# Kernel optimization log

Measured on AMD Instinct MI355X. Metric: run time of the kernel, lower is better.

The kernel has to match this reference:

```python
import jax, jax.numpy as jnp
import numpy as np

N_NODES = 50000
NEG_SLOPE = 0.2  # PyG GATConv default
EPS = 1e-16      # PyG softmax denominator epsilon


def gat_conv(x, W, att_src, att_dst, bias, src, dst, heads, out_ch):
    # x: [N, F_in]; W: [F_in, heads*out_ch]; att_*: [heads, out_ch]
    N = x.shape[0]
    h = (x @ W).reshape(N, heads, out_ch)              # [N,H,C]
    a_src = jnp.sum(h * att_src, axis=-1)              # [N,H]
    a_dst = jnp.sum(h * att_dst, axis=-1)              # [N,H]
    alpha = a_src[src] + a_dst[dst]                    # [E,H]
    alpha = jnp.where(alpha > 0, alpha, NEG_SLOPE * alpha)  # leaky_relu
    amax = jax.ops.segment_max(alpha, dst, num_segments=N)  # [N,H]
    amax = jnp.where(jnp.isfinite(amax), amax, 0.0)
    ex = jnp.exp(alpha - amax[dst])                    # [E,H]
    denom = jax.ops.segment_sum(ex, dst, num_segments=N)    # [N,H]
    coef = ex / (denom[dst] + EPS)                     # [E,H]
    msg = h[src] * coef[:, :, None]                    # [E,H,C]
    out = jax.ops.segment_sum(msg, dst, num_segments=N)     # [N,H,C]
    return out.reshape(N, heads * out_ch) + bias


def setup_inputs() -> dict:
    key = jax.random.key(0)
    ks = jax.random.split(key, 11)
    T, N, F = 8, N_NODES, 64
    E = 1_600_000
    x = jax.random.normal(ks[0], (T, N, F), dtype=jnp.float32)
    edge_index = jax.random.randint(ks[1], (2, E), 0, N, dtype=jnp.int64)
    s = 0.1
    return {
        "x": x,
        "edge_index": edge_index,
        "W1": jax.random.normal(ks[2], (F, 64), jnp.float32) * s,
        "att_src1": jax.random.normal(ks[3], (8, 8), jnp.float32) * s,
        "att_dst1": jax.random.normal(ks[4], (8, 8), jnp.float32) * s,
        "bias1": jax.random.normal(ks[5], (64,), jnp.float32) * s,
        "W2": jax.random.normal(ks[6], (64, F), jnp.float32) * s,
        "att_src2": jax.random.normal(ks[7], (1, F), jnp.float32) * s,
        "att_dst2": jax.random.normal(ks[8], (1, F), jnp.float32) * s,
        "bias2": jax.random.normal(ks[9], (F,), jnp.float32) * s,
    }


def reference(x, edge_index, W1, att_src1, att_dst1, bias1, W2, att_src2, att_dst2, bias2):
    N = x.shape[1]
    # PyG GATConv adds self-loops by default
    loops = jnp.arange(N, dtype=edge_index.dtype)
    src = jnp.concatenate([edge_index[0], loops])
    dst = jnp.concatenate([edge_index[1], loops])

    def step(xt):  # xt: [N, F] ; dropout is identity in eval mode
        y = jax.nn.elu(gat_conv(xt, W1, att_src1, att_dst1, bias1, src, dst, 8, 8))
        y = gat_conv(y, W2, att_src2, att_dst2, bias2, src, dst, 1, xt.shape[-1])
        return jax.nn.log_softmax(y, axis=-1)

    return jax.vmap(step)(x)  # [T, N, F]
```

## Files before the change

kernel.cpp:

```cpp
#include <hip/hip_runtime.h>
#include <hip/hip_bf16.h>
#include <math.h>


typedef __hip_bfloat16 bf16;

__device__ __forceinline__ float bf2f(unsigned short u) {
    return __uint_as_float(((unsigned int)u) << 16);
}


__global__ __launch_bounds__(256) void count_edges_kernel(const int* __restrict__ dsts,
                                                          int* cnt, int E) {
    int i = blockIdx.x * 256 + threadIdx.x;
    if (i < E) atomicAdd(&cnt[dsts[i]], 1);
}

__global__ __launch_bounds__(1024) void scan_kernel(const int* __restrict__ cnt,
                                                    int* row, int* cur, int N) {
    __shared__ int ls[1024];
    int t = threadIdx.x;
    int chunk = (N + 1023) / 1024;
    int b = t * chunk;
    int sum = 0;
    for (int i = 0; i < chunk; ++i) {
        int idx = b + i;
        if (idx < N) sum += cnt[idx] + 1;
    }
    ls[t] = sum;
    __syncthreads();
    for (int off = 1; off < 1024; off <<= 1) {
        int v = (t >= off) ? ls[t - off] : 0;
        __syncthreads();
        ls[t] += v;
        __syncthreads();
    }
    int run = (t == 0) ? 0 : ls[t - 1];
    for (int i = 0; i < chunk; ++i) {
        int idx = b + i;
        if (idx < N) {
            int c = cnt[idx] + 1;
            row[idx] = run;
            cur[idx] = run;
            run += c;
        }
    }
    if (t == 1023) row[N] = ls[1023];
}

__global__ __launch_bounds__(256) void fill_csr_kernel(const int* __restrict__ srcs,
                                                       const int* __restrict__ dsts,
                                                       int* cur, int* esrc, int E, int N) {
    int i = blockIdx.x * 256 + threadIdx.x;
    if (i >= E + N) return;
    int s, d;
    if (i < E) { s = srcs[i]; d = dsts[i]; }
    else       { s = i - E;   d = s; }
    int pos = atomicAdd(&cur[d], 1);
    esrc[pos] = s;
}


__device__ __forceinline__ float4 ld4(const float* p) { return *(const float4*)p; }
__device__ __forceinline__ float4 ld4(const bf16* p) {
    ushort4 u = *(const ushort4*)p;
    float4 r;
    r.x = bf2f(u.x); r.y = bf2f(u.y); r.z = bf2f(u.z); r.w = bf2f(u.w);
    return r;
}


template <typename TIN, int H, int C>
__global__ __launch_bounds__(256) void gemm_att_kernel(
    const TIN* __restrict__ xin,
    size_t node_stride, size_t t_stride,
    const float* __restrict__ Wm,
    const float* __restrict__ att_s,
    const float* __restrict__ att_d,
    bf16* __restrict__ hout,
    float* __restrict__ asrc,
    float* __restrict__ adst,
    int N) {
    __shared__ float Ws[64 * 64];
    int tid = threadIdx.x;
    {
        const float4* W4 = (const float4*)Wm;
        float4* Ws4 = (float4*)Ws;
#pragma unroll
        for (int i = 0; i < 4; ++i) Ws4[tid + 256 * i] = W4[tid + 256 * i];
    }
    __syncthreads();

    int c  = tid & 63;
    int wv = tid >> 6;
    int t0 = blockIdx.y * 4;
    int n  = blockIdx.x * 4 + wv;
    if (n >= N) return;

    const TIN* xb = xin + (size_t)n * node_stride + (size_t)t0 * t_stride;
    float acc[4] = {0.f, 0.f, 0.f, 0.f};

#pragma unroll 2
    for (int k4 = 0; k4 < 16; ++k4) {
        float4 xv[4];
#pragma unroll
        for (int r = 0; r < 4; ++r)
            xv[r] = ld4(xb + (size_t)r * t_stride + k4 * 4);
        float w0 = Ws[(4 * k4 + 0) * 64 + c];
        float w1 = Ws[(4 * k4 + 1) * 64 + c];
        float w2 = Ws[(4 * k4 + 2) * 64 + c];
        float w3 = Ws[(4 * k4 + 3) * 64 + c];
#pragma unroll
        for (int r = 0; r < 4; ++r) {
            acc[r] = fmaf(xv[r].x, w0, acc[r]);
            acc[r] = fmaf(xv[r].y, w1, acc[r]);
            acc[r] = fmaf(xv[r].z, w2, acc[r]);
            acc[r] = fmaf(xv[r].w, w3, acc[r]);
        }
    }

    float as_w = att_s[c];
    float ad_w = att_d[c];
    bf16*  hn  = hout + (size_t)n * 512;
    float* asn = asrc + (size_t)n * (8 * H);
    float* adn = adst + (size_t)n * (8 * H);
#pragma unroll
    for (int r = 0; r < 4; ++r) {
        int tt = t0 + r;
        float a = acc[r];
        hn[tt * 64 + c] = __float2bfloat16(a);
        float vs = a * as_w;
        float vd = a * ad_w;
#pragma unroll
        for (int off = 1; off < C; off <<= 1) {
            vs += __shfl_xor(vs, off, 64);
            vd += __shfl_xor(vd, off, 64);
        }
        if ((c % C) == 0) {
            int hd = c / C;
            asn[tt * H + hd] = vs;
            adn[tt * H + hd] = vd;
        }
    }
}


#define SWZ(PU, Q) __uint_as_float(__builtin_amdgcn_ds_swizzle((PU), ((Q) << 5) | 0x18))

template <int H, bool FINAL>
__global__ __launch_bounds__(256) void gat_edge_kernel(
    const bf16* __restrict__ h_all,
    const float* __restrict__ asrc_all,
    const float* __restrict__ adst_all,
    const int* __restrict__ row,
    const int* __restrict__ esrc,
    const float* __restrict__ bias,
    bf16* __restrict__ outb,
    float* __restrict__ outf,
    int N) {
    int tid  = threadIdx.x;
    int lane = tid & 63;
    int t0   = blockIdx.y * 4;
    int n    = blockIdx.x * 4 + (tid >> 6);
    if (n >= N) return;

    const char* asrcb = (const char*)asrc_all;
    const unsigned short* hb = (const unsigned short*)h_all;

    const int head = (H == 8) ? (lane >> 3) : 0;
    float adn[4];
#pragma unroll
    for (int i = 0; i < 4; ++i)
        adn[i] = adst_all[(size_t)n * (8 * H) + (t0 + i) * H + head];

    int e0  = row[n];
    int deg = row[n + 1] - e0;
    int toff = t0 * 64 + lane;

    float lsum[4] = {0.f, 0.f, 0.f, 0.f};
    float acc[4]  = {0.f, 0.f, 0.f, 0.f};

    for (int base = 0; base < deg; base += 64) {
        int cnt = deg - base; if (cnt > 64) cnt = 64;
        int sv = (lane < cnt) ? esrc[e0 + base + lane] : 0;

        if constexpr (H == 8) {
            unsigned head4 = (unsigned)(head << 2);
            unsigned l7_4  = (unsigned)((lane & 7) << 2);
#pragma unroll
            for (int sub = 0; sub < 8; ++sub) {
                if (sub * 8 >= cnt) break;
                int svj = __builtin_amdgcn_ds_bpermute(sub * 32 + l7_4, sv);
                unsigned abase = (((unsigned)svj) << 8) | head4;
                bool valid = (sub * 8 + (lane & 7) < cnt);
                float p[4];
#pragma unroll
                for (int i = 0; i < 4; ++i) {
                    float av = *(const float*)(asrcb + (abase | ((unsigned)(t0 + i) << 5)));
                    float tv = av + adn[i];
                    tv = tv > 0.f ? tv : 0.2f * tv;
                    tv = valid ? tv : -INFINITY;
                    p[i] = __expf(tv);
                    lsum[i] += p[i];
                }
                unsigned pu0 = __float_as_uint(p[0]);
                unsigned pu1 = __float_as_uint(p[1]);
                unsigned pu2 = __float_as_uint(p[2]);
                unsigned pu3 = __float_as_uint(p[3]);
#define ACC_EDGE(Q)                                                            \
    {                                                                          \
        unsigned sj = (unsigned)__builtin_amdgcn_readlane(sv, sub * 8 + (Q));  \
        const unsigned short* hrow = hb + ((size_t)sj << 9) + toff;            \
        acc[0] = fmaf(SWZ(pu0, Q), bf2f(hrow[0]),   acc[0]);                   \
        acc[1] = fmaf(SWZ(pu1, Q), bf2f(hrow[64]),  acc[1]);                   \
        acc[2] = fmaf(SWZ(pu2, Q), bf2f(hrow[128]), acc[2]);                   \
        acc[3] = fmaf(SWZ(pu3, Q), bf2f(hrow[192]), acc[3]);                   \
    }
                ACC_EDGE(0) ACC_EDGE(1) ACC_EDGE(2) ACC_EDGE(3)
                ACC_EDGE(4) ACC_EDGE(5) ACC_EDGE(6) ACC_EDGE(7)
#undef ACC_EDGE
            }
        } else {
            unsigned abase = ((unsigned)sv) << 5;
            float p[4];
#pragma unroll
            for (int i = 0; i < 4; ++i) {
                float av = *(const float*)(asrcb + (abase | ((unsigned)(t0 + i) << 2)));
                float tv = av + adn[i];
                tv = tv > 0.f ? tv : 0.2f * tv;
                tv = (lane < cnt) ? tv : -INFINITY;
                p[i] = __expf(tv);
                lsum[i] += p[i];
            }
            for (int j0 = 0; j0 < cnt; j0 += 8) {
#pragma unroll
                for (int q = 0; q < 8; ++q) {
                    int j = j0 + q;
                    unsigned sj = (unsigned)__builtin_amdgcn_readlane(sv, j);
                    const unsigned short* hrow = hb + ((size_t)sj << 9) + toff;
                    float pj0 = __uint_as_float(
                        __builtin_amdgcn_readlane(__float_as_uint(p[0]), j));
                    float pj1 = __uint_as_float(
                        __builtin_amdgcn_readlane(__float_as_uint(p[1]), j));
                    float pj2 = __uint_as_float(
                        __builtin_amdgcn_readlane(__float_as_uint(p[2]), j));
                    float pj3 = __uint_as_float(
                        __builtin_amdgcn_readlane(__float_as_uint(p[3]), j));
                    acc[0] = fmaf(pj0, bf2f(hrow[0]),   acc[0]);
                    acc[1] = fmaf(pj1, bf2f(hrow[64]),  acc[1]);
                    acc[2] = fmaf(pj2, bf2f(hrow[128]), acc[2]);
                    acc[3] = fmaf(pj3, bf2f(hrow[192]), acc[3]);
                }
            }
        }
    }

#pragma unroll
    for (int i = 0; i < 4; ++i) {
        float ls = lsum[i];
        if constexpr (H == 8) {
            ls += __shfl_xor(ls, 1, 64);
            ls += __shfl_xor(ls, 2, 64);
            ls += __shfl_xor(ls, 4, 64);
        } else {
#pragma unroll
            for (int o = 1; o < 64; o <<= 1) ls += __shfl_xor(ls, o, 64);
        }
        float v = acc[i] / (ls + 1e-16f) + bias[lane];
        if (!FINAL) {
            float y = v > 0.f ? v : expm1f(v);
            outb[(size_t)n * 512 + (t0 + i) * 64 + lane] = __float2bfloat16(y);
        } else {
            float mx = v;
#pragma unroll
            for (int off = 1; off < 64; off <<= 1) mx = fmaxf(mx, __shfl_xor(mx, off, 64));
            float ex = __expf(v - mx);
            float sm = ex;
#pragma unroll
            for (int off = 1; off < 64; off <<= 1) sm += __shfl_xor(sm, off, 64);
            outf[(size_t)(t0 + i) * N * 64 + (size_t)n * 64 + lane] =
                (v - mx) - __logf(sm);
        }
    }
}


extern "C" void kernel_launch(void* const* d_in, const int* in_sizes, int n_in,
                              void* d_out, int out_size, void* d_ws, size_t ws_size,
                              hipStream_t stream) {
    const float* x        = (const float*)d_in[0];
    const int*   eidx     = (const int*)d_in[1];
    const float* W1       = (const float*)d_in[2];
    const float* att_src1 = (const float*)d_in[3];
    const float* att_dst1 = (const float*)d_in[4];
    const float* bias1    = (const float*)d_in[5];
    const float* W2       = (const float*)d_in[6];
    const float* att_src2 = (const float*)d_in[7];
    const float* att_dst2 = (const float*)d_in[8];
    const float* bias2    = (const float*)d_in[9];
    float* dout = (float*)d_out;

    const int N = 50000;
    const int F = 64;
    const int E = in_sizes[1] / 2;
    const int T = in_sizes[0] / (N * F);
    const int NT = T * N;
    const int Etot = E + N;
    const int BPT = (N + 3) / 4;

    const int* srcs = eidx;
    const int* dsts = eidx + E;

    char* ws = (char*)d_ws;
    size_t off = 0;
    auto carve = [&](size_t bytes) -> void* {
        void* p = ws + off;
        off = (off + bytes + 255) & ~(size_t)255;
        return p;
    };
    bf16*  h_all  = (bf16*)carve((size_t)NT * 64 * sizeof(bf16));
    bf16*  y1_all = (bf16*)carve((size_t)NT * 64 * sizeof(bf16));
    float* asrc   = (float*)carve((size_t)NT * 8 * sizeof(float));
    float* adst   = (float*)carve((size_t)NT * 8 * sizeof(float));
    int*   rowp   = (int*)carve((size_t)(N + 1) * sizeof(int));
    int*   cnt    = (int*)carve((size_t)N * sizeof(int));
    int*   cur    = (int*)carve((size_t)N * sizeof(int));
    int*   esrc   = (int*)carve((size_t)Etot * sizeof(int));
    (void)ws_size;

    hipMemsetAsync(cnt, 0, (size_t)N * sizeof(int), stream);
    count_edges_kernel<<<(E + 255) / 256, 256, 0, stream>>>(dsts, cnt, E);
    scan_kernel<<<1, 1024, 0, stream>>>(cnt, rowp, cur, N);
    fill_csr_kernel<<<(E + N + 255) / 256, 256, 0, stream>>>(srcs, dsts, cur, esrc, E, N);

    dim3 ggrid((N + 3) / 4, 2);
    dim3 egrid(BPT, T / 4);
    gemm_att_kernel<float, 8, 8><<<ggrid, 256, 0, stream>>>(
        x, 64, (size_t)N * 64, W1, att_src1, att_dst1, h_all, asrc, adst, N);
    gat_edge_kernel<8, false><<<egrid, 256, 0, stream>>>(
        h_all, asrc, adst, rowp, esrc, bias1, y1_all, nullptr, N);
    gemm_att_kernel<bf16, 1, 64><<<ggrid, 256, 0, stream>>>(
        y1_all, 512, 64, W2, att_src2, att_dst2, h_all, asrc, adst, N);
    gat_edge_kernel<1, true><<<egrid, 256, 0, stream>>>(
        h_all, asrc, adst, rowp, esrc, bias2, nullptr, dout, N);
}
```

Measured before the change: 1.144 ms.

## Interleave timesteps in h layout and process all 8 timesteps per wave

The GEMM kernel now stores h as [node][channel][timestep] and attention scores as [node][head][timestep], so each lane loads one 16-byte vector per edge holding all 8 timesteps of its channel. The edge kernel drops the timestep grid dimension and handles all 8 timesteps in one wave. This halves the number of CSR traversals, esrc reads and readlanes per edge, and replaces scattered 2-byte gathers with 16-byte ones. The cost is doubled accumulator and probability register pressure, which may lower occupancy, and half as many blocks in flight.

```diff
diff --git a/kernel.cpp b/kernel.cpp
--- a/kernel.cpp
+++ b/kernel.cpp
@@ -7,6 +7,16 @@
 
 __device__ __forceinline__ float bf2f(unsigned short u) {
     return __uint_as_float(((unsigned int)u) << 16);
+}
+__device__ __forceinline__ float lo16(int u) {
+    return __uint_as_float(((unsigned)u) << 16);
+}
+__device__ __forceinline__ float hi16(int u) {
+    return __uint_as_float(((unsigned)u) & 0xFFFF0000u);
+}
+__device__ __forceinline__ unsigned short f2bfu(float f) {
+    bf16 b = __float2bfloat16(f);
+    return *reinterpret_cast<unsigned short*>(&b);
 }
 
 
@@ -119,16 +129,22 @@
         }
     }
 
+    {
+        unsigned short* hn = (unsigned short*)hout + (size_t)n * 512;
+        ushort4 hv;
+        hv.x = f2bfu(acc[0]); hv.y = f2bfu(acc[1]);
+        hv.z = f2bfu(acc[2]); hv.w = f2bfu(acc[3]);
+        *(ushort4*)(hn + c * 8 + t0) = hv;
+    }
+
     float as_w = att_s[c];
     float ad_w = att_d[c];
-    bf16*  hn  = hout + (size_t)n * 512;
-    float* asn = asrc + (size_t)n * (8 * H);
-    float* adn = adst + (size_t)n * (8 * H);
+    float* asn = asrc + (size_t)n * (H * 8);
+    float* adn = adst + (size_t)n * (H * 8);
 #pragma unroll
     for (int r = 0; r < 4; ++r) {
         int tt = t0 + r;
         float a = acc[r];
-        hn[tt * 64 + c] = __float2bfloat16(a);
         float vs = a * as_w;
         float vd = a * ad_w;
 #pragma unroll
@@ -138,8 +154,8 @@
         }
         if ((c % C) == 0) {
             int hd = c / C;
-            asn[tt * H + hd] = vs;
-            adn[tt * H + hd] = vd;
+            asn[hd * 8 + tt] = vs;
+            adn[hd * 8 + tt] = vd;
         }
     }
 }
@@ -160,104 +176,114 @@
     int N) {
     int tid  = threadIdx.x;
     int lane = tid & 63;
-    int t0   = blockIdx.y * 4;
     int n    = blockIdx.x * 4 + (tid >> 6);
     if (n >= N) return;
 
-    const char* asrcb = (const char*)asrc_all;
     const unsigned short* hb = (const unsigned short*)h_all;
-
     const int head = (H == 8) ? (lane >> 3) : 0;
-    float adn[4];
-#pragma unroll
-    for (int i = 0; i < 4; ++i)
-        adn[i] = adst_all[(size_t)n * (8 * H) + (t0 + i) * H + head];
+
+    float adn[8];
+    {
+        const float* adp = adst_all + (size_t)n * (H * 8) + (head << 3);
+        float4 d0 = ld4(adp), d1 = ld4(adp + 4);
+        adn[0] = d0.x; adn[1] = d0.y; adn[2] = d0.z; adn[3] = d0.w;
+        adn[4] = d1.x; adn[5] = d1.y; adn[6] = d1.z; adn[7] = d1.w;
+    }
 
     int e0  = row[n];
     int deg = row[n + 1] - e0;
-    int toff = t0 * 64 + lane;
-
-    float lsum[4] = {0.f, 0.f, 0.f, 0.f};
-    float acc[4]  = {0.f, 0.f, 0.f, 0.f};
+
+    float lsum[8] = {0.f, 0.f, 0.f, 0.f, 0.f, 0.f, 0.f, 0.f};
+    float acc[8]  = {0.f, 0.f, 0.f, 0.f, 0.f, 0.f, 0.f, 0.f};
 
     for (int base = 0; base < deg; base += 64) {
         int cnt = deg - base; if (cnt > 64) cnt = 64;
         int sv = (lane < cnt) ? esrc[e0 + base + lane] : 0;
 
         if constexpr (H == 8) {
-            unsigned head4 = (unsigned)(head << 2);
-            unsigned l7_4  = (unsigned)((lane & 7) << 2);
+            unsigned l7_4 = (unsigned)((lane & 7) << 2);
 #pragma unroll
             for (int sub = 0; sub < 8; ++sub) {
                 if (sub * 8 >= cnt) break;
                 int svj = __builtin_amdgcn_ds_bpermute(sub * 32 + l7_4, sv);
-                unsigned abase = (((unsigned)svj) << 8) | head4;
+                const float* ap = asrc_all + ((size_t)(unsigned)svj << 6) + (head << 3);
+                float4 a0 = ld4(ap), a1 = ld4(ap + 4);
                 bool valid = (sub * 8 + (lane & 7) < cnt);
-                float p[4];
-#pragma unroll
-                for (int i = 0; i < 4; ++i) {
-                    float av = *(const float*)(asrcb + (abase | ((unsigned)(t0 + i) << 5)));
-                    float tv = av + adn[i];
+                float at[8] = {a0.x, a0.y, a0.z, a0.w, a1.x, a1.y, a1.z, a1.w};
+                float p[8];
+#pragma unroll
+                for (int t = 0; t < 8; ++t) {
+                    float tv = at[t] + adn[t];
                     tv = tv > 0.f ? tv : 0.2f * tv;
                     tv = valid ? tv : -INFINITY;
-                    p[i] = __expf(tv);
-                    lsum[i] += p[i];
+                    p[t] = __expf(tv);
+                    lsum[t] += p[t];
                 }
-                unsigned pu0 = __float_as_uint(p[0]);
-                unsigned pu1 = __float_as_uint(p[1]);
-                unsigned pu2 = __float_as_uint(p[2]);
-                unsigned pu3 = __float_as_uint(p[3]);
+                unsigned pu0 = __float_as_uint(p[0]), pu1 = __float_as_uint(p[1]);
+                unsigned pu2 = __float_as_uint(p[2]), pu3 = __float_as_uint(p[3]);
+                unsigned pu4 = __float_as_uint(p[4]), pu5 = __float_as_uint(p[5]);
+                unsigned pu6 = __float_as_uint(p[6]), pu7 = __float_as_uint(p[7]);
 #define ACC_EDGE(Q)                                                            \
     {                                                                          \
         unsigned sj = (unsigned)__builtin_amdgcn_readlane(sv, sub * 8 + (Q));  \
-        const unsigned short* hrow = hb + ((size_t)sj << 9) + toff;            \
-        acc[0] = fmaf(SWZ(pu0, Q), bf2f(hrow[0]),   acc[0]);                   \
-        acc[1] = fmaf(SWZ(pu1, Q), bf2f(hrow[64]),  acc[1]);                   \
-        acc[2] = fmaf(SWZ(pu2, Q), bf2f(hrow[128]), acc[2]);                   \
-        acc[3] = fmaf(SWZ(pu3, Q), bf2f(hrow[192]), acc[3]);                   \
+        int4 hv = ((const int4*)(hb + ((size_t)sj << 9)))[lane];               \
+        acc[0] = fmaf(SWZ(pu0, Q), lo16(hv.x), acc[0]);                        \
+        acc[1] = fmaf(SWZ(pu1, Q), hi16(hv.x), acc[1]);                        \
+        acc[2] = fmaf(SWZ(pu2, Q), lo16(hv.y), acc[2]);                        \
+        acc[3] = fmaf(SWZ(pu3, Q), hi16(hv.y), acc[3]);                        \
+        acc[4] = fmaf(SWZ(pu4, Q), lo16(hv.z), acc[4]);                        \
+        acc[5] = fmaf(SWZ(pu5, Q), hi16(hv.z), acc[5]);                        \
+        acc[6] = fmaf(SWZ(pu6, Q), lo16(hv.w), acc[6]);                        \
+        acc[7] = fmaf(SWZ(pu7, Q), hi16(hv.w), acc[7]);                        \
     }
                 ACC_EDGE(0) ACC_EDGE(1) ACC_EDGE(2) ACC_EDGE(3)
                 ACC_EDGE(4) ACC_EDGE(5) ACC_EDGE(6) ACC_EDGE(7)
 #undef ACC_EDGE
             }
         } else {
-            unsigned abase = ((unsigned)sv) << 5;
-            float p[4];
-#pragma unroll
-            for (int i = 0; i < 4; ++i) {
-                float av = *(const float*)(asrcb + (abase | ((unsigned)(t0 + i) << 2)));
-                float tv = av + adn[i];
+            const float* ap = asrc_all + ((size_t)(unsigned)sv << 3);
+            float4 a0 = ld4(ap), a1 = ld4(ap + 4);
+            float at[8] = {a0.x, a0.y, a0.z, a0.w, a1.x, a1.y, a1.z, a1.w};
+            float p[8];
+#pragma unroll
+            for (int t = 0; t < 8; ++t) {
+                float tv = at[t] + adn[t];
                 tv = tv > 0.f ? tv : 0.2f * tv;
                 tv = (lane < cnt) ? tv : -INFINITY;
-                p[i] = __expf(tv);
-                lsum[i] += p[i];
+                p[t] = __expf(tv);
+                lsum[t] += p[t];
             }
             for (int j0 = 0; j0 < cnt; j0 += 8) {
 #pragma unroll
                 for (int q = 0; q < 8; ++q) {
                     int j = j0 + q;
                     unsigned sj = (unsigned)__builtin_amdgcn_readlane(sv, j);
-                    const unsigned short* hrow = hb + ((size_t)sj << 9) + toff;
-                    float pj0 = __uint_as_float(
-                        __builtin_amdgcn_readlane(__float_as_uint(p[0]), j));
-                    float pj1 = __uint_as_float(
-                        __builtin_amdgcn_readlane(__float_as_uint(p[1]), j));
-                    float pj2 = __uint_as_float(
-                        __builtin_amdgcn_readlane(__float_as_uint(p[2]), j));
-                    float pj3 = __uint_as_float(
-                        __builtin_amdgcn_readlane(__float_as_uint(p[3]), j));
-                    acc[0] = fmaf(pj0, bf2f(hrow[0]),   acc[0]);
-                    acc[1] = fmaf(pj1, bf2f(hrow[64]),  acc[1]);
-                    acc[2] = fmaf(pj2, bf2f(hrow[128]), acc[2]);
-                    acc[3] = fmaf(pj3, bf2f(hrow[192]), acc[3]);
+                    int4 hv = ((const int4*)(hb + ((size_t)sj << 9)))[lane];
+                    float pj0 = __uint_as_float(__builtin_amdgcn_readlane(__float_as_uint(p[0]), j));
+                    float pj1 = __uint_as_float(__builtin_amdgcn_readlane(__float_as_uint(p[1]), j));
+                    float pj2 = __uint_as_float(__builtin_amdgcn_readlane(__float_as_uint(p[2]), j));
+                    float pj3 = __uint_as_float(__builtin_amdgcn_readlane(__float_as_uint(p[3]), j));
+                    float pj4 = __uint_as_float(__builtin_amdgcn_readlane(__float_as_uint(p[4]), j));
+                    float pj5 = __uint_as_float(__builtin_amdgcn_readlane(__float_as_uint(p[5]), j));
+                    float pj6 = __uint_as_float(__builtin_amdgcn_readlane(__float_as_uint(p[6]), j));
+                    float pj7 = __uint_as_float(__builtin_amdgcn_readlane(__float_as_uint(p[7]), j));
+                    acc[0] = fmaf(pj0, lo16(hv.x), acc[0]);
+                    acc[1] = fmaf(pj1, hi16(hv.x), acc[1]);
+                    acc[2] = fmaf(pj2, lo16(hv.y), acc[2]);
+                    acc[3] = fmaf(pj3, hi16(hv.y), acc[3]);
+                    acc[4] = fmaf(pj4, lo16(hv.z), acc[4]);
+                    acc[5] = fmaf(pj5, hi16(hv.z), acc[5]);
+                    acc[6] = fmaf(pj6, lo16(hv.w), acc[6]);
+                    acc[7] = fmaf(pj7, hi16(hv.w), acc[7]);
                 }
             }
         }
     }
 
-#pragma unroll
-    for (int i = 0; i < 4; ++i) {
-        float ls = lsum[i];
+    float bi = bias[lane];
+#pragma unroll
+    for (int t = 0; t < 8; ++t) {
+        float ls = lsum[t];
         if constexpr (H == 8) {
             ls += __shfl_xor(ls, 1, 64);
             ls += __shfl_xor(ls, 2, 64);
@@ -266,10 +292,10 @@
 #pragma unroll
             for (int o = 1; o < 64; o <<= 1) ls += __shfl_xor(ls, o, 64);
         }
-        float v = acc[i] / (ls + 1e-16f) + bias[lane];
+        float v = acc[t] / (ls + 1e-16f) + bi;
         if (!FINAL) {
             float y = v > 0.f ? v : expm1f(v);
-            outb[(size_t)n * 512 + (t0 + i) * 64 + lane] = __float2bfloat16(y);
+            outb[(size_t)n * 512 + t * 64 + lane] = __float2bfloat16(y);
         } else {
             float mx = v;
 #pragma unroll
@@ -278,7 +304,7 @@
             float sm = ex;
 #pragma unroll
             for (int off = 1; off < 64; off <<= 1) sm += __shfl_xor(sm, off, 64);
-            outf[(size_t)(t0 + i) * N * 64 + (size_t)n * 64 + lane] =
+            outf[(size_t)t * N * 64 + (size_t)n * 64 + lane] =
                 (v - mx) - __logf(sm);
         }
     }
@@ -334,13 +360,12 @@
     fill_csr_kernel<<<(E + N + 255) / 256, 256, 0, stream>>>(srcs, dsts, cur, esrc, E, N);
 
     dim3 ggrid((N + 3) / 4, 2);
-    dim3 egrid(BPT, T / 4);
     gemm_att_kernel<float, 8, 8><<<ggrid, 256, 0, stream>>>(
         x, 64, (size_t)N * 64, W1, att_src1, att_dst1, h_all, asrc, adst, N);
-    gat_edge_kernel<8, false><<<egrid, 256, 0, stream>>>(
+    gat_edge_kernel<8, false><<<BPT, 256, 0, stream>>>(
         h_all, asrc, adst, rowp, esrc, bias1, y1_all, nullptr, N);
     gemm_att_kernel<bf16, 1, 64><<<ggrid, 256, 0, stream>>>(
         y1_all, 512, 64, W2, att_src2, att_dst2, h_all, asrc, adst, N);
-    gat_edge_kernel<1, true><<<egrid, 256, 0, stream>>>(
+    gat_edge_kernel<1, true><<<BPT, 256, 0, stream>>>(
         h_all, asrc, adst, rowp, esrc, bias2, nullptr, dout, N);
 }
```

New measurement: 1.199 ms. 4.8% more time.

## Sort CSR neighbor lists by source tile for better gather locality

Applied to the files above, without the earlier changes.

Builds the CSR with a two-level bucket per destination: edges are grouped into 16 source-node tiles of 4096 nodes, so each node's neighbor list is roughly ordered by source range. The aim is better cache locality when the edge kernels gather h[src] and a_src. The scan becomes a three-kernel multi-block scan over N*16 buckets, which adds launches, more atomics targets and memory for the count arrays.

```diff
diff --git a/kernel.cpp b/kernel.cpp
--- a/kernel.cpp
+++ b/kernel.cpp
@@ -5,27 +5,52 @@
 
 typedef __hip_bfloat16 bf16;
 
+#define TILES  16
+#define TSHIFT 12
+
 __device__ __forceinline__ float bf2f(unsigned short u) {
     return __uint_as_float(((unsigned int)u) << 16);
 }
 
 
-__global__ __launch_bounds__(256) void count_edges_kernel(const int* __restrict__ dsts,
-                                                          int* cnt, int E) {
+__global__ __launch_bounds__(256) void count2_kernel(const int* __restrict__ srcs,
+                                                     const int* __restrict__ dsts,
+                                                     int* cnt2, int E) {
     int i = blockIdx.x * 256 + threadIdx.x;
-    if (i < E) atomicAdd(&cnt[dsts[i]], 1);
-}
-
-__global__ __launch_bounds__(1024) void scan_kernel(const int* __restrict__ cnt,
-                                                    int* row, int* cur, int N) {
+    if (i < E) atomicAdd(&cnt2[dsts[i] * TILES + (srcs[i] >> TSHIFT)], 1);
+}
+
+__device__ __forceinline__ int bucket_val(const int* __restrict__ cnt2, int idx, int M) {
+    if (idx >= M) return 0;
+    int n = idx >> 4, tile = idx & (TILES - 1);
+    return cnt2[idx] + ((tile == (n >> TSHIFT)) ? 1 : 0);
+}
+
+__global__ __launch_bounds__(256) void scanA_kernel(const int* __restrict__ cnt2,
+                                                    int* bsum, int M) {
+    __shared__ int sd[256];
+    int tid = threadIdx.x;
+    int idx = blockIdx.x * 256 + tid;
+    int v = bucket_val(cnt2, idx, M);
+    sd[tid] = v;
+    __syncthreads();
+    for (int off = 128; off > 0; off >>= 1) {
+        if (tid < off) sd[tid] += sd[tid + off];
+        __syncthreads();
+    }
+    if (tid == 0) bsum[blockIdx.x] = sd[0];
+}
+
+__global__ __launch_bounds__(1024) void scanB_kernel(const int* __restrict__ bsum,
+                                                     int* boff, int B) {
     __shared__ int ls[1024];
     int t = threadIdx.x;
-    int chunk = (N + 1023) / 1024;
+    int chunk = (B + 1023) / 1024;
     int b = t * chunk;
     int sum = 0;
     for (int i = 0; i < chunk; ++i) {
         int idx = b + i;
-        if (idx < N) sum += cnt[idx] + 1;
+        if (idx < B) sum += bsum[idx];
     }
     ls[t] = sum;
     __syncthreads();
@@ -38,25 +63,46 @@
     int run = (t == 0) ? 0 : ls[t - 1];
     for (int i = 0; i < chunk; ++i) {
         int idx = b + i;
-        if (idx < N) {
-            int c = cnt[idx] + 1;
-            row[idx] = run;
-            cur[idx] = run;
-            run += c;
-        }
-    }
-    if (t == 1023) row[N] = ls[1023];
-}
-
-__global__ __launch_bounds__(256) void fill_csr_kernel(const int* __restrict__ srcs,
-                                                       const int* __restrict__ dsts,
-                                                       int* cur, int* esrc, int E, int N) {
+        if (idx < B) {
+            boff[idx] = run;
+            run += bsum[idx];
+        }
+    }
+}
+
+__global__ __launch_bounds__(256) void scanC_kernel(const int* __restrict__ cnt2,
+                                                    const int* __restrict__ boff,
+                                                    int* cur2, int* rowp, int M, int N) {
+    __shared__ int sd[256];
+    int tid = threadIdx.x;
+    int idx = blockIdx.x * 256 + tid;
+    int v = bucket_val(cnt2, idx, M);
+    sd[tid] = v;
+    __syncthreads();
+    for (int off = 1; off < 256; off <<= 1) {
+        int t = (tid >= off) ? sd[tid - off] : 0;
+        __syncthreads();
+        sd[tid] += t;
+        __syncthreads();
+    }
+    int inc = sd[tid];
+    int go  = boff[blockIdx.x] + inc - v;
+    if (idx < M) {
+        cur2[idx] = go;
+        if ((idx & (TILES - 1)) == 0) rowp[idx >> 4] = go;
+        if (idx == M - 1) rowp[N] = go + v;
+    }
+}
+
+__global__ __launch_bounds__(256) void fill2_kernel(const int* __restrict__ srcs,
+                                                    const int* __restrict__ dsts,
+                                                    int* cur2, int* esrc, int E, int N) {
     int i = blockIdx.x * 256 + threadIdx.x;
     if (i >= E + N) return;
     int s, d;
     if (i < E) { s = srcs[i]; d = dsts[i]; }
     else       { s = i - E;   d = s; }
-    int pos = atomicAdd(&cur[d], 1);
+    int pos = atomicAdd(&cur2[d * TILES + (s >> TSHIFT)], 1);
     esrc[pos] = s;
 }
 
@@ -307,6 +353,8 @@
     const int NT = T * N;
     const int Etot = E + N;
     const int BPT = (N + 3) / 4;
+    const int M  = N * TILES;
+    const int SB = (M + 255) / 256;
 
     const int* srcs = eidx;
     const int* dsts = eidx + E;
@@ -323,15 +371,19 @@
     float* asrc   = (float*)carve((size_t)NT * 8 * sizeof(float));
     float* adst   = (float*)carve((size_t)NT * 8 * sizeof(float));
     int*   rowp   = (int*)carve((size_t)(N + 1) * sizeof(int));
-    int*   cnt    = (int*)carve((size_t)N * sizeof(int));
-    int*   cur    = (int*)carve((size_t)N * sizeof(int));
+    int*   cnt2   = (int*)carve((size_t)M * sizeof(int));
+    int*   cur2   = (int*)carve((size_t)M * sizeof(int));
+    int*   bsum   = (int*)carve((size_t)SB * sizeof(int));
+    int*   boff   = (int*)carve((size_t)SB * sizeof(int));
     int*   esrc   = (int*)carve((size_t)Etot * sizeof(int));
     (void)ws_size;
 
-    hipMemsetAsync(cnt, 0, (size_t)N * sizeof(int), stream);
-    count_edges_kernel<<<(E + 255) / 256, 256, 0, stream>>>(dsts, cnt, E);
-    scan_kernel<<<1, 1024, 0, stream>>>(cnt, rowp, cur, N);
-    fill_csr_kernel<<<(E + N + 255) / 256, 256, 0, stream>>>(srcs, dsts, cur, esrc, E, N);
+    hipMemsetAsync(cnt2, 0, (size_t)M * sizeof(int), stream);
+    count2_kernel<<<(E + 255) / 256, 256, 0, stream>>>(srcs, dsts, cnt2, E);
+    scanA_kernel<<<SB, 256, 0, stream>>>(cnt2, bsum, M);
+    scanB_kernel<<<1, 1024, 0, stream>>>(bsum, boff, SB);
+    scanC_kernel<<<SB, 256, 0, stream>>>(cnt2, boff, cur2, rowp, M, N);
+    fill2_kernel<<<(E + N + 255) / 256, 256, 0, stream>>>(srcs, dsts, cur2, esrc, E, N);
 
     dim3 ggrid((N + 3) / 4, 2);
     dim3 egrid(BPT, T / 4);
```

Measured after the change: 1.068 ms. 1.07x faster.
